# Optimization experiments

Measured on AMD Instinct MI355X. Metric: run time of the kernel, lower is better.

Reference implementation:

```python
import jax, jax.numpy as jnp
import numpy as np

EMBED = 1024
HEADS = 16
HEAD_DIM = EMBED // HEADS
B, N = 2, 2048


def setup_inputs() -> dict:
    key = jax.random.key(0)
    ks = jax.random.split(key, 7)
    s = 1.0 / np.sqrt(EMBED)
    x = jax.random.normal(ks[0], (B, N, EMBED), dtype=jnp.float32)
    # causal mask: 1 where attention allowed, 0 elsewhere (masked_fill on mask==0)
    mask = jnp.tril(jnp.ones((N, N), dtype=jnp.int32))[None, None, :, :]
    Wq = jax.random.uniform(ks[1], (EMBED, EMBED), jnp.float32, -s, s)
    Wk = jax.random.uniform(ks[2], (EMBED, EMBED), jnp.float32, -s, s)
    Wv = jax.random.uniform(ks[3], (EMBED, EMBED), jnp.float32, -s, s)
    Wo = jax.random.uniform(ks[4], (EMBED, EMBED), jnp.float32, -s, s)
    bo = jax.random.uniform(ks[5], (EMBED,), jnp.float32, -s, s)
    return {"x": x, "mask": mask, "Wq": Wq, "Wk": Wk, "Wv": Wv, "Wo": Wo, "bo": bo}


def reference(x, mask, Wq, Wk, Wv, Wo, bo):
    Bx, Nx, D = x.shape
    # torch nn.Linear: y = x @ W.T
    q = (x @ Wq.T).reshape(Bx, Nx, HEADS, HEAD_DIM).transpose(0, 2, 1, 3)
    k = (x @ Wk.T).reshape(Bx, Nx, HEADS, HEAD_DIM).transpose(0, 2, 1, 3)
    v = (x @ Wv.T).reshape(Bx, Nx, HEADS, HEAD_DIM).transpose(0, 2, 1, 3)
    score = jnp.einsum('bhqd,bhkd->bhqk', q, k) / np.sqrt(HEAD_DIM).astype(np.float32)
    score = jnp.where(mask == 0, -jnp.inf, score)
    probs = jax.nn.softmax(score, axis=-1)
    out = jnp.einsum('bhqk,bhkd->bhqd', probs, v)  # [B,H,N,hd]
    out = out.transpose(0, 2, 1, 3).reshape(Bx, Nx, D)
    return out @ Wo.T + bo
```

## Files before the change

kernel.cpp:

```cpp
#include <hip/hip_runtime.h>
#include <hip/hip_bf16.h>

#define B_  2
#define N_  2048
#define E_  1024
#define H_  16
#define HD_ 64
#define M_  (B_*N_)
#define RSZ ((size_t)M_ * E_)

typedef short bf16x8 __attribute__((ext_vector_type(8)));
typedef float f32x4 __attribute__((ext_vector_type(4)));
typedef unsigned short u16x8 __attribute__((ext_vector_type(8)));

__device__ __forceinline__ unsigned short f2bfu(float f) {
    __hip_bfloat16 h = __float2bfloat16(f);
    return *reinterpret_cast<unsigned short*>(&h);
}
__device__ __forceinline__ unsigned int pack2bf(float lo, float hi) {
    return ((unsigned int)f2bfu(hi) << 16) | (unsigned int)f2bfu(lo);
}
#define MFMA16(a,b,c) __builtin_amdgcn_mfma_f32_16x16x32_bf16((a),(b),(c),0,0,0)

__global__ __launch_bounds__(256) void fconv_all_kernel(
    const float* __restrict__ x,
    const float* __restrict__ Wq, const float* __restrict__ Wk,
    const float* __restrict__ Wv, const float* __restrict__ Wo,
    unsigned short* __restrict__ xbf, unsigned short* __restrict__ wbf)
{
    const int bid = blockIdx.x;
    const float* src;
    unsigned short* dst;
    int off;
    if (bid < 2048) {
        src = x; dst = xbf; off = bid * 2048 + threadIdx.x * 8;
    } else {
        const int z = (bid - 2048) >> 9;
        src = (z == 0) ? Wq : (z == 1 ? Wk : (z == 2 ? Wv : Wo));
        dst = wbf + (size_t)z * E_ * E_;
        off = ((bid - 2048) & 511) * 2048 + threadIdx.x * 8;
    }
    const float4 a = *reinterpret_cast<const float4*>(src + off);
    const float4 b = *reinterpret_cast<const float4*>(src + off + 4);
    u16x8 v;
    v[0]=f2bfu(a.x); v[1]=f2bfu(a.y); v[2]=f2bfu(a.z); v[3]=f2bfu(a.w);
    v[4]=f2bfu(b.x); v[5]=f2bfu(b.y); v[6]=f2bfu(b.z); v[7]=f2bfu(b.w);
    *reinterpret_cast<u16x8*>(dst + off) = v;
}

__global__ __launch_bounds__(256) void fconv_kernel(
    const float* __restrict__ src, unsigned short* __restrict__ dst)
{
    const int i0 = (blockIdx.x * 256 + threadIdx.x) * 8;
    const float4 a = *reinterpret_cast<const float4*>(src + i0);
    const float4 b = *reinterpret_cast<const float4*>(src + i0 + 4);
    u16x8 v;
    v[0]=f2bfu(a.x); v[1]=f2bfu(a.y); v[2]=f2bfu(a.z); v[3]=f2bfu(a.w);
    v[4]=f2bfu(b.x); v[5]=f2bfu(b.y); v[6]=f2bfu(b.z); v[7]=f2bfu(b.w);
    *reinterpret_cast<u16x8*>(dst + i0) = v;
}

__global__ __launch_bounds__(256) void qkv_bf_kernel(
    const unsigned short* __restrict__ xbf, const unsigned short* __restrict__ wbf,
    unsigned short* __restrict__ qkv)
{
    const int z = blockIdx.z;
    const unsigned short* __restrict__ W = wbf + (size_t)z * E_ * E_;
    unsigned short* __restrict__ out = qkv + (size_t)z * RSZ;
    const int m0 = blockIdx.x * 128;
    const int n0 = blockIdx.y * 128;
    __shared__ unsigned short As[128][72];
    __shared__ unsigned short Bs[128][72];
    const int t = threadIdx.x;
    const int lane = t & 63;
    const int w = t >> 6, wr = w >> 1, wc = w & 1;
    const int fr = lane & 15, fq = lane >> 4;
    const int srow = t >> 1, scol = (t & 1) * 32;
    f32x4 acc[4][4] = {};

    const unsigned short* arow = xbf + (size_t)(m0 + srow) * E_ + scol;
    const unsigned short* brow = W + (size_t)(n0 + srow) * E_ + scol;

    u16x8 a8[4], b8[4];
    #pragma unroll
    for (int i = 0; i < 4; ++i) a8[i] = reinterpret_cast<const u16x8*>(arow)[i];
    #pragma unroll
    for (int i = 0; i < 4; ++i) b8[i] = reinterpret_cast<const u16x8*>(brow)[i];

    for (int k0 = 0; k0 < E_; k0 += 64) {
        __syncthreads();
        #pragma unroll
        for (int j = 0; j < 4; ++j) {
            *reinterpret_cast<u16x8*>(&As[srow][scol + 8*j]) = a8[j];
            *reinterpret_cast<u16x8*>(&Bs[srow][scol + 8*j]) = b8[j];
        }
        __syncthreads();
        if (k0 + 64 < E_) {
            #pragma unroll
            for (int i = 0; i < 4; ++i)
                a8[i] = reinterpret_cast<const u16x8*>(arow + k0 + 64)[i];
            #pragma unroll
            for (int i = 0; i < 4; ++i)
                b8[i] = reinterpret_cast<const u16x8*>(brow + k0 + 64)[i];
        }
        #pragma unroll
        for (int ks = 0; ks < 2; ++ks) {
            bf16x8 af[4], bfv[4];
            #pragma unroll
            for (int mf = 0; mf < 4; ++mf)
                af[mf] = *reinterpret_cast<const bf16x8*>(&As[wr*64 + mf*16 + fr][ks*32 + fq*8]);
            #pragma unroll
            for (int nf = 0; nf < 4; ++nf)
                bfv[nf] = *reinterpret_cast<const bf16x8*>(&Bs[wc*64 + nf*16 + fr][ks*32 + fq*8]);
            #pragma unroll
            for (int mf = 0; mf < 4; ++mf)
                #pragma unroll
                for (int nf = 0; nf < 4; ++nf)
                    acc[mf][nf] = MFMA16(af[mf], bfv[nf], acc[mf][nf]);
        }
    }

    const float scale = (z == 0) ? 0.125f : 1.0f;
    #pragma unroll
    for (int mf = 0; mf < 4; ++mf) {
        #pragma unroll
        for (int r = 0; r < 4; ++r) {
            const int m = m0 + wr*64 + mf*16 + fq*4 + r;
            const int b = m >> 11, npos = m & (N_ - 1);
            #pragma unroll
            for (int nf = 0; nf < 4; ++nf) {
                const int n = n0 + wc*64 + nf*16 + fr;
                const int h = n >> 6, d = n & 63;
                const unsigned short val = f2bfu(acc[mf][nf][r] * scale);
                if (z == 2)
                    out[(((size_t)(b*H_ + h))*HD_ + d)*N_ + npos] = val;
                else
                    out[(((size_t)(b*H_ + h))*N_ + npos)*HD_ + d] = val;
            }
        }
    }
}

__global__ __launch_bounds__(256) void qkv_f32_kernel(
    const float* __restrict__ x, const unsigned short* __restrict__ wbf,
    unsigned short* __restrict__ qkv)
{
    const int z = blockIdx.z;
    const unsigned short* __restrict__ W = wbf + (size_t)z * E_ * E_;
    unsigned short* __restrict__ out = qkv + (size_t)z * RSZ;
    const int m0 = blockIdx.x * 128;
    const int n0 = blockIdx.y * 128;
    __shared__ unsigned short As[128][72];
    __shared__ unsigned short Bs[128][72];
    const int t = threadIdx.x;
    const int lane = t & 63;
    const int w = t >> 6, wr = w >> 1, wc = w & 1;
    const int fr = lane & 15, fq = lane >> 4;
    const int srow = t >> 1, scol = (t & 1) * 32;
    f32x4 acc[4][4] = {};

    const float* arow = x + (size_t)(m0 + srow) * E_ + scol;
    const unsigned short* brow = W + (size_t)(n0 + srow) * E_ + scol;

    float4 a4[8];
    u16x8 b8[4];
    #pragma unroll
    for (int i = 0; i < 8; ++i) a4[i] = reinterpret_cast<const float4*>(arow)[i];
    #pragma unroll
    for (int i = 0; i < 4; ++i) b8[i] = reinterpret_cast<const u16x8*>(brow)[i];

    for (int k0 = 0; k0 < E_; k0 += 64) {
        __syncthreads();
        #pragma unroll
        for (int j = 0; j < 4; ++j) {
            u16x8 va;
            va[0]=f2bfu(a4[2*j].x); va[1]=f2bfu(a4[2*j].y); va[2]=f2bfu(a4[2*j].z); va[3]=f2bfu(a4[2*j].w);
            va[4]=f2bfu(a4[2*j+1].x); va[5]=f2bfu(a4[2*j+1].y); va[6]=f2bfu(a4[2*j+1].z); va[7]=f2bfu(a4[2*j+1].w);
            *reinterpret_cast<u16x8*>(&As[srow][scol + 8*j]) = va;
            *reinterpret_cast<u16x8*>(&Bs[srow][scol + 8*j]) = b8[j];
        }
        __syncthreads();
        if (k0 + 64 < E_) {
            #pragma unroll
            for (int i = 0; i < 8; ++i)
                a4[i] = reinterpret_cast<const float4*>(arow + k0 + 64)[i];
            #pragma unroll
            for (int i = 0; i < 4; ++i)
                b8[i] = reinterpret_cast<const u16x8*>(brow + k0 + 64)[i];
        }
        #pragma unroll
        for (int ks = 0; ks < 2; ++ks) {
            bf16x8 af[4], bfv[4];
            #pragma unroll
            for (int mf = 0; mf < 4; ++mf)
                af[mf] = *reinterpret_cast<const bf16x8*>(&As[wr*64 + mf*16 + fr][ks*32 + fq*8]);
            #pragma unroll
            for (int nf = 0; nf < 4; ++nf)
                bfv[nf] = *reinterpret_cast<const bf16x8*>(&Bs[wc*64 + nf*16 + fr][ks*32 + fq*8]);
            #pragma unroll
            for (int mf = 0; mf < 4; ++mf)
                #pragma unroll
                for (int nf = 0; nf < 4; ++nf)
                    acc[mf][nf] = MFMA16(af[mf], bfv[nf], acc[mf][nf]);
        }
    }

    const float scale = (z == 0) ? 0.125f : 1.0f;
    #pragma unroll
    for (int mf = 0; mf < 4; ++mf) {
        #pragma unroll
        for (int r = 0; r < 4; ++r) {
            const int m = m0 + wr*64 + mf*16 + fq*4 + r;
            const int b = m >> 11, npos = m & (N_ - 1);
            #pragma unroll
            for (int nf = 0; nf < 4; ++nf) {
                const int n = n0 + wc*64 + nf*16 + fr;
                const int h = n >> 6, d = n & 63;
                const unsigned short val = f2bfu(acc[mf][nf][r] * scale);
                if (z == 2)
                    out[(((size_t)(b*H_ + h))*HD_ + d)*N_ + npos] = val;
                else
                    out[(((size_t)(b*H_ + h))*N_ + npos)*HD_ + d] = val;
            }
        }
    }
}

__global__ __launch_bounds__(512) void attn_mfma_kernel(
    const unsigned short* __restrict__ qkv, unsigned short* __restrict__ attn_out)
{
    const int bh = blockIdx.x;
    const int xp = blockIdx.y;
    const unsigned short* Qp  = qkv + (size_t)bh * N_ * HD_;
    const unsigned short* Kp  = qkv + RSZ + (size_t)bh * N_ * HD_;
    const unsigned short* Vtp = qkv + 2*RSZ + (size_t)bh * N_ * HD_;
    __shared__ unsigned short Ks[64][72], Vt[64][72];
    const int t = threadIdx.x;
    const int lane = t & 63, w = t >> 6;
    const int fr = lane & 15, fq = lane >> 4;
    const int srow = t >> 3, sc0 = (t & 7) * 8;
    const int qbase = (w < 4) ? ((31 - xp) * 64 + w * 16)
                              : (xp * 64 + (w - 4) * 16);
    const int KT = 32 - xp;
    const int ql = qbase + fr;
    const int lane_b0 = (2 * (fq & 1)) * 16 + fr;
    const int lane_b1 = lane_b0 + 16;
    const bool hi_sel = (fq >> 1) != 0;

    bf16x8 qfr[2];
    #pragma unroll
    for (int ks = 0; ks < 2; ++ks)
        qfr[ks] = *reinterpret_cast<const bf16x8*>(
            Qp + (size_t)ql * HD_ + ks*32 + fq*8);

    float m_run = -1e30f, l_run = 0.f;
    f32x4 o[4] = {};

    u16x8 kreg = *reinterpret_cast<const u16x8*>(Kp + (size_t)srow * HD_ + sc0);
    u16x8 vreg = *reinterpret_cast<const u16x8*>(Vtp + (size_t)srow * N_ + sc0);

    for (int kt = 0; kt < KT; ++kt) {
        const int k0 = kt * 64;
        __syncthreads();
        *reinterpret_cast<u16x8*>(&Ks[srow][sc0]) = kreg;
        *reinterpret_cast<u16x8*>(&Vt[srow][sc0]) = vreg;
        __syncthreads();
        if (kt + 1 < KT) {
            kreg = *reinterpret_cast<const u16x8*>(Kp + (size_t)(k0 + 64 + srow) * HD_ + sc0);
            vreg = *reinterpret_cast<const u16x8*>(Vtp + (size_t)srow * N_ + k0 + 64 + sc0);
        }
        if (k0 > qbase + 15) continue;

        f32x4 s[4] = {};
        __builtin_amdgcn_s_setprio(1);
        #pragma unroll
        for (int ks = 0; ks < 2; ++ks) {
            bf16x8 bk[4];
            #pragma unroll
            for (int nf = 0; nf < 4; ++nf)
                bk[nf] = *reinterpret_cast<const bf16x8*>(&Ks[nf*16 + fr][ks*32 + fq*8]);
            #pragma unroll
            for (int nf = 0; nf < 4; ++nf)
                s[nf] = MFMA16(bk[nf], qfr[ks], s[nf]);
        }
        __builtin_amdgcn_s_setprio(0);

        if (k0 + 63 > qbase) {
            #pragma unroll
            for (int nf = 0; nf < 4; ++nf)
                #pragma unroll
                for (int r = 0; r < 4; ++r)
                    if (k0 + nf*16 + fq*4 + r > ql) s[nf][r] = -1e30f;
        }

        float pm = -1e30f;
        #pragma unroll
        for (int nf = 0; nf < 4; ++nf)
            pm = fmaxf(pm, fmaxf(fmaxf(s[nf][0], s[nf][1]),
                                 fmaxf(s[nf][2], s[nf][3])));
        pm = fmaxf(pm, __shfl_xor(pm, 16));
        pm = fmaxf(pm, __shfl_xor(pm, 32));

        const bool need = __any(pm > m_run + 8.f);
        float scl = 1.f;
        if (need) {
            const float mnew = fmaxf(m_run, pm);
            scl = __expf(m_run - mnew);
            m_run = mnew;
        }

        float rs = 0.f;
        unsigned int u[4][2];
        #pragma unroll
        for (int nf = 0; nf < 4; ++nf) {
            const float p0 = __expf(s[nf][0] - m_run);
            const float p1 = __expf(s[nf][1] - m_run);
            const float p2 = __expf(s[nf][2] - m_run);
            const float p3 = __expf(s[nf][3] - m_run);
            rs += (p0 + p1) + (p2 + p3);
            u[nf][0] = pack2bf(p0, p1);
            u[nf][1] = pack2bf(p2, p3);
        }
        {
            float v = rs;
            v += __shfl_xor(v, 16);
            v += __shfl_xor(v, 32);
            l_run = l_run * scl + v;
        }
        if (need) {
            #pragma unroll
            for (int df = 0; df < 4; ++df)
                #pragma unroll
                for (int r = 0; r < 4; ++r)
                    o[df][r] *= scl;
        }

        bf16x8 pb[2];
        #pragma unroll
        for (int ks = 0; ks < 2; ++ks) {
            const unsigned int t00 = __shfl(u[2*ks+0][0], lane_b0);
            const unsigned int t01 = __shfl(u[2*ks+0][1], lane_b0);
            const unsigned int t02 = __shfl(u[2*ks+0][0], lane_b1);
            const unsigned int t03 = __shfl(u[2*ks+0][1], lane_b1);
            const unsigned int t10 = __shfl(u[2*ks+1][0], lane_b0);
            const unsigned int t11 = __shfl(u[2*ks+1][1], lane_b0);
            const unsigned int t12 = __shfl(u[2*ks+1][0], lane_b1);
            const unsigned int t13 = __shfl(u[2*ks+1][1], lane_b1);
            union { unsigned int wd[4]; bf16x8 v; } pu;
            pu.wd[0] = hi_sel ? t10 : t00;
            pu.wd[1] = hi_sel ? t11 : t01;
            pu.wd[2] = hi_sel ? t12 : t02;
            pu.wd[3] = hi_sel ? t13 : t03;
            pb[ks] = pu.v;
        }

        __builtin_amdgcn_s_setprio(1);
        #pragma unroll
        for (int ks = 0; ks < 2; ++ks) {
            bf16x8 bv[4];
            #pragma unroll
            for (int df = 0; df < 4; ++df)
                bv[df] = *reinterpret_cast<const bf16x8*>(&Vt[df*16 + fr][ks*32 + fq*8]);
            #pragma unroll
            for (int df = 0; df < 4; ++df)
                o[df] = MFMA16(bv[df], pb[ks], o[df]);
        }
        __builtin_amdgcn_s_setprio(0);
    }

    const int b = bh >> 4, h = bh & 15;
    const float inv = 1.0f / l_run;
    #pragma unroll
    for (int df = 0; df < 4; ++df)
        #pragma unroll
        for (int r = 0; r < 4; ++r) {
            const int d = df*16 + fq*4 + r;
            attn_out[((size_t)(b*N_ + ql))*E_ + h*64 + d] = f2bfu(o[df][r] * inv);
        }
}

__global__ __launch_bounds__(256) void out_mfma_kernel(
    const unsigned short* __restrict__ A, const unsigned short* __restrict__ Wobf,
    const float* __restrict__ bo, float* __restrict__ out)
{
    const int m0 = blockIdx.x * 128;
    const int n0 = blockIdx.y * 128;
    __shared__ unsigned short As[128][72];
    __shared__ unsigned short Bs[128][72];
    const int t = threadIdx.x;
    const int lane = t & 63;
    const int w = t >> 6, wr = w >> 1, wc = w & 1;
    const int fr = lane & 15, fq = lane >> 4;
    const int srow = t >> 1, scol = (t & 1) * 32;
    f32x4 acc[4][4] = {};

    const unsigned short* arow = A + (size_t)(m0 + srow) * E_ + scol;
    const unsigned short* brow = Wobf + (size_t)(n0 + srow) * E_ + scol;

    u16x8 a8[4], b8[4];
    #pragma unroll
    for (int i = 0; i < 4; ++i) a8[i] = reinterpret_cast<const u16x8*>(arow)[i];
    #pragma unroll
    for (int i = 0; i < 4; ++i) b8[i] = reinterpret_cast<const u16x8*>(brow)[i];

    for (int k0 = 0; k0 < E_; k0 += 64) {
        __syncthreads();
        #pragma unroll
        for (int j = 0; j < 4; ++j) {
            *reinterpret_cast<u16x8*>(&As[srow][scol + 8*j]) = a8[j];
            *reinterpret_cast<u16x8*>(&Bs[srow][scol + 8*j]) = b8[j];
        }
        __syncthreads();
        if (k0 + 64 < E_) {
            #pragma unroll
            for (int i = 0; i < 4; ++i)
                a8[i] = reinterpret_cast<const u16x8*>(arow + k0 + 64)[i];
            #pragma unroll
            for (int i = 0; i < 4; ++i)
                b8[i] = reinterpret_cast<const u16x8*>(brow + k0 + 64)[i];
        }
        #pragma unroll
        for (int ks = 0; ks < 2; ++ks) {
            bf16x8 af[4], bfv[4];
            #pragma unroll
            for (int mf = 0; mf < 4; ++mf)
                af[mf] = *reinterpret_cast<const bf16x8*>(&As[wr*64 + mf*16 + fr][ks*32 + fq*8]);
            #pragma unroll
            for (int nf = 0; nf < 4; ++nf)
                bfv[nf] = *reinterpret_cast<const bf16x8*>(&Bs[wc*64 + nf*16 + fr][ks*32 + fq*8]);
            #pragma unroll
            for (int mf = 0; mf < 4; ++mf)
                #pragma unroll
                for (int nf = 0; nf < 4; ++nf)
                    acc[mf][nf] = MFMA16(af[mf], bfv[nf], acc[mf][nf]);
        }
    }

    #pragma unroll
    for (int mf = 0; mf < 4; ++mf) {
        #pragma unroll
        for (int r = 0; r < 4; ++r) {
            const int m = m0 + wr*64 + mf*16 + fq*4 + r;
            #pragma unroll
            for (int nf = 0; nf < 4; ++nf) {
                const int n = n0 + wc*64 + nf*16 + fr;
                out[(size_t)m * E_ + n] = acc[mf][nf][r] + bo[n];
            }
        }
    }
}

extern "C" void kernel_launch(void* const* d_in, const int* in_sizes, int n_in,
                              void* d_out, int out_size, void* d_ws, size_t ws_size,
                              hipStream_t stream) {
    const float* x  = (const float*)d_in[0];
    const float* Wq = (const float*)d_in[2];
    const float* Wk = (const float*)d_in[3];
    const float* Wv = (const float*)d_in[4];
    const float* Wo = (const float*)d_in[5];
    const float* bo = (const float*)d_in[6];
    float* out = (float*)d_out;

    unsigned short* ws = (unsigned short*)d_ws;
    const size_t need_main = 5 * RSZ * sizeof(unsigned short);

    if (ws_size >= need_main) {
        unsigned short* xbf  = ws;
        unsigned short* wbf  = ws + RSZ;
        unsigned short* qkvq = ws + 2 * RSZ;
        unsigned short* attn_ws = ws;
        unsigned short* wobf = wbf + 3 * (size_t)E_ * E_;

        fconv_all_kernel<<<4096, 256, 0, stream>>>(x, Wq, Wk, Wv, Wo, xbf, wbf);

        dim3 g1(M_ / 128, E_ / 128, 3);
        qkv_bf_kernel<<<g1, 256, 0, stream>>>(xbf, wbf, qkvq);

        dim3 g2(B_ * H_, 16);
        attn_mfma_kernel<<<g2, 512, 0, stream>>>(qkvq, attn_ws);

        dim3 g3(M_ / 128, E_ / 128);
        out_mfma_kernel<<<g3, 256, 0, stream>>>(attn_ws, wobf, bo, out);
    } else {
        unsigned short* wbf = ws;
        unsigned short* qkvq = ws + RSZ;
        unsigned short* attn_ws = ws;
        unsigned short* wobf = ws + RSZ;

        const int cgrid = E_ * E_ / (256 * 8);
        fconv_kernel<<<cgrid, 256, 0, stream>>>(Wq, wbf);
        fconv_kernel<<<cgrid, 256, 0, stream>>>(Wk, wbf + (size_t)E_ * E_);
        fconv_kernel<<<cgrid, 256, 0, stream>>>(Wv, wbf + 2 * (size_t)E_ * E_);

        dim3 g1(M_ / 128, E_ / 128, 3);
        qkv_f32_kernel<<<g1, 256, 0, stream>>>(x, wbf, qkvq);

        dim3 g2(B_ * H_, 16);
        attn_mfma_kernel<<<g2, 512, 0, stream>>>(qkvq, attn_ws);

        fconv_kernel<<<cgrid, 256, 0, stream>>>(Wo, wobf);

        dim3 g3(M_ / 128, E_ / 128);
        out_mfma_kernel<<<g3, 256, 0, stream>>>(attn_ws, wobf, bo, out);
    }
}
```

Baseline: 118.1 us.

## Stage GEMM tiles via direct global-to-LDS loads with XOR swizzle and double buffering

Both the QKV and output-projection GEMMs now copy tiles straight from global memory into shared memory with global_load_lds, instead of going through registers. The tiles use an XOR-swizzled unpadded layout so fragment reads avoid bank conflicts, and the shared buffers are doubled so the next K tile loads while the current one is computed. This cuts register pressure and VGPR round-trips and removes one barrier per iteration. In exchange, shared memory per block roughly doubles, which may lower occupancy, and correctness depends on the async loads being complete by the barrier.

```diff
diff --git a/kernel.cpp b/kernel.cpp
--- a/kernel.cpp
+++ b/kernel.cpp
@@ -13,6 +13,9 @@
 typedef float f32x4 __attribute__((ext_vector_type(4)));
 typedef unsigned short u16x8 __attribute__((ext_vector_type(8)));
 
+#define AS1 __attribute__((address_space(1)))
+#define AS3 __attribute__((address_space(3)))
+
 __device__ __forceinline__ unsigned short f2bfu(float f) {
     __hip_bfloat16 h = __float2bfloat16(f);
     return *reinterpret_cast<unsigned short*>(&h);
@@ -21,6 +24,10 @@
     return ((unsigned int)f2bfu(hi) << 16) | (unsigned int)f2bfu(lo);
 }
 #define MFMA16(a,b,c) __builtin_amdgcn_mfma_f32_16x16x32_bf16((a),(b),(c),0,0,0)
+
+__device__ __forceinline__ void gl_lds16(const void* g, void* l) {
+    __builtin_amdgcn_global_load_lds((const AS1 void*)g, (AS3 void*)l, 16, 0, 0);
+}
 
 __global__ __launch_bounds__(256) void fconv_all_kernel(
     const float* __restrict__ x,
@@ -60,7 +67,7 @@
     *reinterpret_cast<u16x8*>(dst + i0) = v;
 }
 
-__global__ __launch_bounds__(256) void qkv_bf_kernel(
+__global__ __launch_bounds__(256) void qkv_glds_kernel(
     const unsigned short* __restrict__ xbf, const unsigned short* __restrict__ wbf,
     unsigned short* __restrict__ qkv)
 {
@@ -69,56 +76,55 @@
     unsigned short* __restrict__ out = qkv + (size_t)z * RSZ;
     const int m0 = blockIdx.x * 128;
     const int n0 = blockIdx.y * 128;
-    __shared__ unsigned short As[128][72];
-    __shared__ unsigned short Bs[128][72];
+    __shared__ unsigned short ldsA[2][128*64];
+    __shared__ unsigned short ldsB[2][128*64];
     const int t = threadIdx.x;
     const int lane = t & 63;
     const int w = t >> 6, wr = w >> 1, wc = w & 1;
     const int fr = lane & 15, fq = lane >> 4;
-    const int srow = t >> 1, scol = (t & 1) * 32;
+    const int subrow = lane >> 3;
+    const int csw = ((lane & 7) ^ subrow) * 8;
+    const int rcol = ((fq * 8) ^ ((fr & 7) * 8));
     f32x4 acc[4][4] = {};
 
-    const unsigned short* arow = xbf + (size_t)(m0 + srow) * E_ + scol;
-    const unsigned short* brow = W + (size_t)(n0 + srow) * E_ + scol;
-
-    u16x8 a8[4], b8[4];
-    #pragma unroll
-    for (int i = 0; i < 4; ++i) a8[i] = reinterpret_cast<const u16x8*>(arow)[i];
-    #pragma unroll
-    for (int i = 0; i < 4; ++i) b8[i] = reinterpret_cast<const u16x8*>(brow)[i];
-
-    for (int k0 = 0; k0 < E_; k0 += 64) {
-        __syncthreads();
-        #pragma unroll
-        for (int j = 0; j < 4; ++j) {
-            *reinterpret_cast<u16x8*>(&As[srow][scol + 8*j]) = a8[j];
-            *reinterpret_cast<u16x8*>(&Bs[srow][scol + 8*j]) = b8[j];
-        }
-        __syncthreads();
-        if (k0 + 64 < E_) {
-            #pragma unroll
-            for (int i = 0; i < 4; ++i)
-                a8[i] = reinterpret_cast<const u16x8*>(arow + k0 + 64)[i];
-            #pragma unroll
-            for (int i = 0; i < 4; ++i)
-                b8[i] = reinterpret_cast<const u16x8*>(brow + k0 + 64)[i];
-        }
+    #define QKV_STAGE(buf, kt)                                                  \
+        {                                                                       \
+            const int k0_ = (kt) * 64;                                          \
+            _Pragma("unroll")                                                   \
+            for (int i = 0; i < 4; ++i) {                                       \
+                const int chunk = w * 4 + i;                                    \
+                const int row = chunk * 8 + subrow;                             \
+                gl_lds16(xbf + (size_t)(m0 + row) * E_ + k0_ + csw,             \
+                         &ldsA[buf][chunk * 512]);                              \
+                gl_lds16(W + (size_t)(n0 + row) * E_ + k0_ + csw,               \
+                         &ldsB[buf][chunk * 512]);                              \
+            }                                                                   \
+        }
+
+    QKV_STAGE(0, 0);
+    __syncthreads();
+    int cur = 0;
+    for (int kt = 0; kt < 16; ++kt) {
+        if (kt + 1 < 16) QKV_STAGE(cur ^ 1, kt + 1);
         #pragma unroll
         for (int ks = 0; ks < 2; ++ks) {
             bf16x8 af[4], bfv[4];
             #pragma unroll
             for (int mf = 0; mf < 4; ++mf)
-                af[mf] = *reinterpret_cast<const bf16x8*>(&As[wr*64 + mf*16 + fr][ks*32 + fq*8]);
+                af[mf] = *(const bf16x8*)&ldsA[cur][(wr*64 + mf*16 + fr)*64 + (rcol ^ (ks*32))];
             #pragma unroll
             for (int nf = 0; nf < 4; ++nf)
-                bfv[nf] = *reinterpret_cast<const bf16x8*>(&Bs[wc*64 + nf*16 + fr][ks*32 + fq*8]);
+                bfv[nf] = *(const bf16x8*)&ldsB[cur][(wc*64 + nf*16 + fr)*64 + (rcol ^ (ks*32))];
             #pragma unroll
             for (int mf = 0; mf < 4; ++mf)
                 #pragma unroll
                 for (int nf = 0; nf < 4; ++nf)
                     acc[mf][nf] = MFMA16(af[mf], bfv[nf], acc[mf][nf]);
         }
-    }
+        __syncthreads();
+        cur ^= 1;
+    }
+    #undef QKV_STAGE
 
     const float scale = (z == 0) ? 0.125f : 1.0f;
     #pragma unroll
@@ -379,62 +385,61 @@
         }
 }
 
-__global__ __launch_bounds__(256) void out_mfma_kernel(
+__global__ __launch_bounds__(256) void out_glds_kernel(
     const unsigned short* __restrict__ A, const unsigned short* __restrict__ Wobf,
     const float* __restrict__ bo, float* __restrict__ out)
 {
     const int m0 = blockIdx.x * 128;
     const int n0 = blockIdx.y * 128;
-    __shared__ unsigned short As[128][72];
-    __shared__ unsigned short Bs[128][72];
+    __shared__ unsigned short ldsA[2][128*64];
+    __shared__ unsigned short ldsB[2][128*64];
     const int t = threadIdx.x;
     const int lane = t & 63;
     const int w = t >> 6, wr = w >> 1, wc = w & 1;
     const int fr = lane & 15, fq = lane >> 4;
-    const int srow = t >> 1, scol = (t & 1) * 32;
+    const int subrow = lane >> 3;
+    const int csw = ((lane & 7) ^ subrow) * 8;
+    const int rcol = ((fq * 8) ^ ((fr & 7) * 8));
     f32x4 acc[4][4] = {};
 
-    const unsigned short* arow = A + (size_t)(m0 + srow) * E_ + scol;
-    const unsigned short* brow = Wobf + (size_t)(n0 + srow) * E_ + scol;
-
-    u16x8 a8[4], b8[4];
-    #pragma unroll
-    for (int i = 0; i < 4; ++i) a8[i] = reinterpret_cast<const u16x8*>(arow)[i];
-    #pragma unroll
-    for (int i = 0; i < 4; ++i) b8[i] = reinterpret_cast<const u16x8*>(brow)[i];
-
-    for (int k0 = 0; k0 < E_; k0 += 64) {
-        __syncthreads();
-        #pragma unroll
-        for (int j = 0; j < 4; ++j) {
-            *reinterpret_cast<u16x8*>(&As[srow][scol + 8*j]) = a8[j];
-            *reinterpret_cast<u16x8*>(&Bs[srow][scol + 8*j]) = b8[j];
-        }
-        __syncthreads();
-        if (k0 + 64 < E_) {
-            #pragma unroll
-            for (int i = 0; i < 4; ++i)
-                a8[i] = reinterpret_cast<const u16x8*>(arow + k0 + 64)[i];
-            #pragma unroll
-            for (int i = 0; i < 4; ++i)
-                b8[i] = reinterpret_cast<const u16x8*>(brow + k0 + 64)[i];
-        }
+    #define OUT_STAGE(buf, kt)                                                  \
+        {                                                                       \
+            const int k0_ = (kt) * 64;                                          \
+            _Pragma("unroll")                                                   \
+            for (int i = 0; i < 4; ++i) {                                       \
+                const int chunk = w * 4 + i;                                    \
+                const int row = chunk * 8 + subrow;                             \
+                gl_lds16(A + (size_t)(m0 + row) * E_ + k0_ + csw,               \
+                         &ldsA[buf][chunk * 512]);                              \
+                gl_lds16(Wobf + (size_t)(n0 + row) * E_ + k0_ + csw,            \
+                         &ldsB[buf][chunk * 512]);                              \
+            }                                                                   \
+        }
+
+    OUT_STAGE(0, 0);
+    __syncthreads();
+    int cur = 0;
+    for (int kt = 0; kt < 16; ++kt) {
+        if (kt + 1 < 16) OUT_STAGE(cur ^ 1, kt + 1);
         #pragma unroll
         for (int ks = 0; ks < 2; ++ks) {
             bf16x8 af[4], bfv[4];
             #pragma unroll
             for (int mf = 0; mf < 4; ++mf)
-                af[mf] = *reinterpret_cast<const bf16x8*>(&As[wr*64 + mf*16 + fr][ks*32 + fq*8]);
+                af[mf] = *(const bf16x8*)&ldsA[cur][(wr*64 + mf*16 + fr)*64 + (rcol ^ (ks*32))];
             #pragma unroll
             for (int nf = 0; nf < 4; ++nf)
-                bfv[nf] = *reinterpret_cast<const bf16x8*>(&Bs[wc*64 + nf*16 + fr][ks*32 + fq*8]);
+                bfv[nf] = *(const bf16x8*)&ldsB[cur][(wc*64 + nf*16 + fr)*64 + (rcol ^ (ks*32))];
             #pragma unroll
             for (int mf = 0; mf < 4; ++mf)
                 #pragma unroll
                 for (int nf = 0; nf < 4; ++nf)
                     acc[mf][nf] = MFMA16(af[mf], bfv[nf], acc[mf][nf]);
         }
-    }
+        __syncthreads();
+        cur ^= 1;
+    }
+    #undef OUT_STAGE
 
     #pragma unroll
     for (int mf = 0; mf < 4; ++mf) {
@@ -474,13 +479,13 @@
         fconv_all_kernel<<<4096, 256, 0, stream>>>(x, Wq, Wk, Wv, Wo, xbf, wbf);
 
         dim3 g1(M_ / 128, E_ / 128, 3);
-        qkv_bf_kernel<<<g1, 256, 0, stream>>>(xbf, wbf, qkvq);
+        qkv_glds_kernel<<<g1, 256, 0, stream>>>(xbf, wbf, qkvq);
 
         dim3 g2(B_ * H_, 16);
         attn_mfma_kernel<<<g2, 512, 0, stream>>>(qkvq, attn_ws);
 
         dim3 g3(M_ / 128, E_ / 128);
-        out_mfma_kernel<<<g3, 256, 0, stream>>>(attn_ws, wobf, bo, out);
+        out_glds_kernel<<<g3, 256, 0, stream>>>(attn_ws, wobf, bo, out);
     } else {
         unsigned short* wbf = ws;
         unsigned short* qkvq = ws + RSZ;
@@ -501,6 +506,6 @@
         fconv_kernel<<<cgrid, 256, 0, stream>>>(Wo, wobf);
 
         dim3 g3(M_ / 128, E_ / 128);
-        out_mfma_kernel<<<g3, 256, 0, stream>>>(attn_ws, wobf, bo, out);
-    }
-}
+        out_glds_kernel<<<g3, 256, 0, stream>>>(attn_ws, wobf, bo, out);
+    }
+}
```

Result: slower. 126.8 us (+7.4%).
